# Kernel optimization log

Hardware: AMD Instinct MI355X
Metric: run time of the kernel (lower is better)

Reference implementation:

```python
import jax, jax.numpy as jnp
import numpy as np

K = 7          # involution kernel size
P = 3          # padding = (K-1)//2
GC = 16        # group_channels in involution
EPS = 1e-5


def bn(x, g, b):
    # training-mode BatchNorm2d forward: per-channel batch stats over (B,H,W)
    m = jnp.mean(x, axis=(0, 2, 3), keepdims=True)
    v = jnp.var(x, axis=(0, 2, 3), keepdims=True)
    return (x - m) * jax.lax.rsqrt(v + EPS) * g[None, :, None, None] + b[None, :, None, None]


def conv1x1(x, w):
    # x: [B,C,H,W], w: [O,C] -> [B,O,H,W]
    return jnp.einsum('bchw,oc->bohw', x, w)


def unfold7(x):
    # torch F.unfold(kernel=7, pad=3, stride=1) -> [B, C, K*K, H, W] (C slowest, matching torch layout)
    B, C, H, W = x.shape
    xp = jnp.pad(x, ((0, 0), (0, 0), (P, P), (P, P)))
    return jnp.stack([xp[:, :, i:i + H, j:j + W] for i in range(K) for j in range(K)], axis=2)


def involution(x, wr, gr, br, ws):
    # kernel generation: 1x1 reduce -> BN -> ReLU -> 1x1 span to G*K*K per-pixel kernels
    B, C, H, W = x.shape
    G = C // GC
    t = jax.nn.relu(bn(conv1x1(x, wr), gr, br))          # [B, C//4, H, W]
    w = conv1x1(t, ws).reshape(B, G, 1, K * K, H, W)     # per-pixel kernels
    p = unfold7(x).reshape(B, G, GC, K * K, H, W)        # unfolded patches
    return jnp.sum(w * p, axis=3).reshape(B, C, H, W)    # multiply-accumulate over K*K


def setup_inputs() -> dict:
    key = jax.random.key(0)
    ks = jax.random.split(key, 14)
    Cin, Cout, mid = 256, 256, 64
    red = mid // 4                 # reduction_ratio = 4
    G = mid // GC                  # groups = 4
    s = lambda *sh: 1.0 / np.sqrt(np.prod(sh[1:]) if len(sh) > 1 else sh[0])
    return {
        'x':  jax.random.normal(ks[0], (8, Cin, 56, 56), jnp.float32),
        'w1': jax.random.normal(ks[1], (mid, Cin), jnp.float32) * s(mid, Cin),
        'g1': jnp.ones((mid,), jnp.float32),
        'b1': jnp.zeros((mid,), jnp.float32),
        'wr': jax.random.normal(ks[2], (red, mid), jnp.float32) * s(red, mid),
        'gr': jnp.ones((red,), jnp.float32),
        'br': jnp.zeros((red,), jnp.float32),
        'ws': jax.random.normal(ks[3], (K * K * G, red), jnp.float32) * s(K * K * G, red),
        'g2': jnp.ones((mid,), jnp.float32),
        'b2': jnp.zeros((mid,), jnp.float32),
        'w3': jax.random.normal(ks[4], (Cout, mid), jnp.float32) * s(Cout, mid),
        'g3': jnp.ones((Cout,), jnp.float32),
        'b3': jnp.zeros((Cout,), jnp.float32),
    }


def reference(x, w1, g1, b1, wr, gr, br, ws, g2, b2, w3, g3, b3):
    out = jax.nn.relu(bn(conv1x1(x, w1), g1, b1))        # conv1 1x1 + BN + ReLU
    out = jax.nn.relu(bn(involution(out, wr, gr, br, ws), g2, b2))  # involution + BN + ReLU
    out = bn(conv1x1(out, w3), g3, b3)                   # conv3 1x1 + BN
    return jax.nn.relu(out + x)                          # residual add + ReLU
```

## Files before the change

### kernel.cpp

```cpp
#include <hip/hip_runtime.h>

#define HW 3136
#define NPIX 25088
#define NBLK 392

#define OFF_Y1   0u
#define OFF_TR   1605632u
#define OFF_WT   2007040u
#define OFF_OUT2 6924288u
#define OFF_Y3   8529920u
#define OFF_ST   14952448u
#define ACC1 0
#define ACCR 128
#define ACC2 160
#define ACC3 288
#define FIN1 800
#define FINR 928
#define FIN2 960
#define FIN3 1088

__device__ __forceinline__ float wave_sum(float v) {
    #pragma unroll
    for (int off = 32; off > 0; off >>= 1) v += __shfl_xor(v, off, 64);
    return v;
}

__global__ __launch_bounds__(256) void k_wt(const float* __restrict__ w1,
        const float* __restrict__ w3, float* __restrict__ w1t, float* __restrict__ w3t) {
    int i = blockIdx.x * 256 + threadIdx.x;
    if (i < 16384) {
        int oc = i >> 8, ic = i & 255;
        w1t[ic * 64 + oc] = w1[i];
    } else {
        int j = i - 16384;
        int oc = j >> 6, ic = j & 63;
        w3t[ic * 256 + oc] = w3[j];
    }
}

__global__ __launch_bounds__(256, 2) void k_conv1(const float* __restrict__ x,
        const float* __restrict__ w1t, float* __restrict__ y1, float* __restrict__ st) {
    __shared__ float ws[256][32];
    int t = threadIdx.x, blk = blockIdx.x;
    int oh = blk & 1, pb = blk >> 1;
    int b = pb / 49, hw0 = (pb % 49) * 64;
    int tx = t & 15, ty = t >> 4;
    #pragma unroll
    for (int i = 0; i < 8; i++) {
        int e = i * 256 + t;
        int ic = e >> 3, c4 = e & 7;
        *(float4*)&ws[ic][c4 * 4] = *(const float4*)&w1t[ic * 64 + oh * 32 + c4 * 4];
    }
    __syncthreads();
    float a00 = 0.f, a01 = 0.f, a02 = 0.f, a03 = 0.f;
    float a10 = 0.f, a11 = 0.f, a12 = 0.f, a13 = 0.f;
    const float* xp = x + (size_t)b * 256 * HW + hw0 + tx * 4;
    #pragma unroll 8
    for (int ic = 0; ic < 256; ic++) {
        float4 xv = *(const float4*)(xp + (size_t)ic * HW);
        float2 wv = *(const float2*)&ws[ic][ty * 2];
        a00 = fmaf(wv.x, xv.x, a00); a01 = fmaf(wv.x, xv.y, a01);
        a02 = fmaf(wv.x, xv.z, a02); a03 = fmaf(wv.x, xv.w, a03);
        a10 = fmaf(wv.y, xv.x, a10); a11 = fmaf(wv.y, xv.y, a11);
        a12 = fmaf(wv.y, xv.z, a12); a13 = fmaf(wv.y, xv.w, a13);
    }
    #pragma unroll
    for (int io = 0; io < 2; io++) {
        int oc = oh * 32 + ty * 2 + io;
        float4 o = io ? make_float4(a10, a11, a12, a13) : make_float4(a00, a01, a02, a03);
        *(float4*)&y1[((b * 64) + oc) * HW + hw0 + tx * 4] = o;
        float s = o.x + o.y + o.z + o.w;
        float q = o.x * o.x + o.y * o.y + o.z * o.z + o.w * o.w;
        #pragma unroll
        for (int off = 1; off <= 8; off <<= 1) {
            s += __shfl_xor(s, off, 64);
            q += __shfl_xor(q, off, 64);
        }
        if (tx == 0) {
            atomicAdd(&st[ACC1 + oc], s);
            atomicAdd(&st[ACC1 + 64 + oc], q);
        }
    }
}

__global__ void k_fin(const float* __restrict__ acc, float* __restrict__ fin,
                      const float* __restrict__ gamma, const float* __restrict__ beta, int C) {
    int c = threadIdx.x;
    if (c < C) {
        float mean = acc[c] * (1.0f / (float)NPIX);
        float var  = acc[C + c] * (1.0f / (float)NPIX) - mean * mean;
        float rstd = rsqrtf(var + 1e-5f);
        float a = gamma[c] * rstd;
        fin[c] = a;
        fin[C + c] = beta[c] - mean * a;
    }
}

__global__ __launch_bounds__(256, 4) void k_bn1_convr(float* __restrict__ y1,
        const float* __restrict__ wr, float* __restrict__ tr, float* __restrict__ st) {
    __shared__ float ys[64][64];
    __shared__ float wsh[16][64];
    int t = threadIdx.x, pb = blockIdx.x;
    int b = pb / 49, hw0 = (pb % 49) * 64;
    int tx = t & 15, ty = t >> 4;
    #pragma unroll
    for (int i = 0; i < 16; i++) {
        int e = i * 256 + t, c = e >> 6, p = e & 63;
        int gi = ((b * 64) + c) * HW + hw0 + p;
        float v = y1[gi];
        v = fmaxf(st[FIN1 + c] * v + st[FIN1 + 64 + c], 0.f);
        ys[c][p] = v;
        y1[gi] = v;
    }
    #pragma unroll
    for (int i = 0; i < 4; i++) {
        int e = i * 256 + t;
        wsh[e >> 6][e & 63] = wr[e];
    }
    __syncthreads();
    float a0 = 0.f, a1 = 0.f, a2 = 0.f, a3 = 0.f;
    #pragma unroll 8
    for (int c = 0; c < 64; c++) {
        float4 yv = *(const float4*)&ys[c][tx * 4];
        float wv = wsh[ty][c];
        a0 = fmaf(wv, yv.x, a0); a1 = fmaf(wv, yv.y, a1);
        a2 = fmaf(wv, yv.z, a2); a3 = fmaf(wv, yv.w, a3);
    }
    *(float4*)&tr[((b * 16) + ty) * HW + hw0 + tx * 4] = make_float4(a0, a1, a2, a3);
    float s = a0 + a1 + a2 + a3;
    float q = a0 * a0 + a1 * a1 + a2 * a2 + a3 * a3;
    #pragma unroll
    for (int off = 1; off <= 8; off <<= 1) {
        s += __shfl_xor(s, off, 64);
        q += __shfl_xor(q, off, 64);
    }
    if (tx == 0) {
        atomicAdd(&st[ACCR + ty], s);
        atomicAdd(&st[ACCR + 16 + ty], q);
    }
}

__global__ __launch_bounds__(256) void k_invol(const float* __restrict__ y1r,
        const float* __restrict__ tr, const float* __restrict__ wsp,
        float* __restrict__ out2, float* __restrict__ st) {
    __shared__ float ts[16][256];
    __shared__ float sw[49][16];
    __shared__ float ps[8][10][64];
    __shared__ float red[4][16];
    int t = threadIdx.x, bidx = blockIdx.x;
    int h = bidx & 1, r2 = bidx >> 1;
    int ht = r2 % 14;
    int bg = r2 / 14;
    int g = bg & 3, b = bg >> 2;
    int h0 = ht * 4;
    int c0 = h * 8;
    #pragma unroll
    for (int i = 0; i < 16; i++) {
        int e = i * 256 + t, c = e >> 8, p = e & 255;
        if (p < 224) {
            float v = tr[((b * 16) + c) * HW + h0 * 56 + p];
            ts[c][p] = fmaxf(st[FINR + c] * v + st[FINR + 16 + c], 0.f);
        }
    }
    for (int e = t; e < 784; e += 256) sw[e >> 4][e & 15] = wsp[g * 784 + e];
    for (int i = 0; i < 20; i++) {
        int e = i * 256 + t;
        int c = e / 640, rem = e - c * 640;
        int r = rem >> 6, wc = rem & 63;
        int gh = h0 + r - 3, gw = wc - 3;
        float v = 0.f;
        if (gh >= 0 && gh < 56 && gw >= 0 && gw < 56)
            v = y1r[((b * 64) + g * 16 + c0 + c) * HW + gh * 56 + gw];
        ps[c][r][wc] = v;
    }
    __syncthreads();
    float accv[8];
    #pragma unroll
    for (int c = 0; c < 8; c++) accv[c] = 0.f;
    bool active = t < 224;
    if (active) {
        int lh = t / 56, lw = t % 56;
        float tsr[16];
        #pragma unroll
        for (int c = 0; c < 16; c++) tsr[c] = ts[c][t];
        float kr[49];
        #pragma unroll
        for (int k = 0; k < 49; k++) {
            const float4* swr = (const float4*)&sw[k][0];
            float4 u0 = swr[0], u1 = swr[1], u2 = swr[2], u3 = swr[3];
            float v = u0.x * tsr[0];
            v = fmaf(u0.y, tsr[1], v);  v = fmaf(u0.z, tsr[2], v);  v = fmaf(u0.w, tsr[3], v);
            v = fmaf(u1.x, tsr[4], v);  v = fmaf(u1.y, tsr[5], v);  v = fmaf(u1.z, tsr[6], v);
            v = fmaf(u1.w, tsr[7], v);  v = fmaf(u2.x, tsr[8], v);  v = fmaf(u2.y, tsr[9], v);
            v = fmaf(u2.z, tsr[10], v); v = fmaf(u2.w, tsr[11], v); v = fmaf(u3.x, tsr[12], v);
            v = fmaf(u3.y, tsr[13], v); v = fmaf(u3.z, tsr[14], v); v = fmaf(u3.w, tsr[15], v);
            kr[k] = v;
        }
        #pragma unroll
        for (int k = 0; k < 49; k++) {
            int ki = k / 7, kj = k % 7;
            float kv = kr[k];
            #pragma unroll
            for (int c = 0; c < 8; c++)
                accv[c] = fmaf(kv, ps[c][lh + ki][lw + kj], accv[c]);
        }
        int hw = h0 * 56 + t;
        #pragma unroll
        for (int c = 0; c < 8; c++)
            out2[((b * 64) + g * 16 + c0 + c) * HW + hw] = accv[c];
    }
    int wave = t >> 6, lane = t & 63;
    #pragma unroll
    for (int c = 0; c < 8; c++) {
        float v = active ? accv[c] : 0.f;
        float s  = wave_sum(v);
        float s2 = wave_sum(v * v);
        if (lane == 0) { red[wave][c] = s; red[wave][8 + c] = s2; }
    }
    __syncthreads();
    if (t < 16) {
        float s = red[0][t] + red[1][t] + red[2][t] + red[3][t];
        int c = t & 7, isq = t >> 3;
        atomicAdd(&st[ACC2 + isq * 64 + g * 16 + c0 + c], s);
    }
}

__global__ __launch_bounds__(256, 4) void k_bn2_conv3(const float* __restrict__ out2,
        const float* __restrict__ w3t, float* __restrict__ y3, float* __restrict__ st) {
    __shared__ float os[64][64];
    __shared__ float wst[64][64];
    int t = threadIdx.x, blk = blockIdx.x;
    int occ = blk & 3, pb = blk >> 2;
    int b = pb / 49, hw0 = (pb % 49) * 64;
    int tx = t & 15, ty = t >> 4;
    #pragma unroll
    for (int i = 0; i < 16; i++) {
        int e = i * 256 + t, c = e >> 6, p = e & 63;
        float v = out2[((b * 64) + c) * HW + hw0 + p];
        os[c][p] = fmaxf(st[FIN2 + c] * v + st[FIN2 + 64 + c], 0.f);
        wst[c][p] = w3t[c * 256 + occ * 64 + p];
    }
    __syncthreads();
    float acc[4][4];
    #pragma unroll
    for (int i = 0; i < 4; i++)
        #pragma unroll
        for (int j = 0; j < 4; j++) acc[i][j] = 0.f;
    #pragma unroll 8
    for (int c = 0; c < 64; c++) {
        float4 xv = *(const float4*)&os[c][tx * 4];
        float4 wv = *(const float4*)&wst[c][ty * 4];
        float xa[4] = {xv.x, xv.y, xv.z, xv.w};
        float wa[4] = {wv.x, wv.y, wv.z, wv.w};
        #pragma unroll
        for (int i = 0; i < 4; i++)
            #pragma unroll
            for (int j = 0; j < 4; j++) acc[i][j] = fmaf(wa[i], xa[j], acc[i][j]);
    }
    #pragma unroll
    for (int i = 0; i < 4; i++) {
        int oc = occ * 64 + ty * 4 + i;
        float4 o = make_float4(acc[i][0], acc[i][1], acc[i][2], acc[i][3]);
        *(float4*)&y3[((b * 256) + oc) * HW + hw0 + tx * 4] = o;
        float s = o.x + o.y + o.z + o.w;
        float q = o.x * o.x + o.y * o.y + o.z * o.z + o.w * o.w;
        #pragma unroll
        for (int off = 1; off <= 8; off <<= 1) {
            s += __shfl_xor(s, off, 64);
            q += __shfl_xor(q, off, 64);
        }
        if (tx == 0) {
            atomicAdd(&st[ACC3 + oc], s);
            atomicAdd(&st[ACC3 + 256 + oc], q);
        }
    }
}

__global__ __launch_bounds__(256) void k_final(const float* __restrict__ y3,
        const float* __restrict__ x, float* __restrict__ out, const float* __restrict__ st) {
    int idx = blockIdx.x * 256 + threadIdx.x;
    if (idx < 1605632) {
        int c = (idx / 784) & 255;
        float a = st[FIN3 + c], bb = st[FIN3 + 256 + c];
        float4 v  = ((const float4*)y3)[idx];
        float4 xv = ((const float4*)x)[idx];
        float4 o;
        o.x = fmaxf(a * v.x + bb + xv.x, 0.f);
        o.y = fmaxf(a * v.y + bb + xv.y, 0.f);
        o.z = fmaxf(a * v.z + bb + xv.z, 0.f);
        o.w = fmaxf(a * v.w + bb + xv.w, 0.f);
        ((float4*)out)[idx] = o;
    }
}

extern "C" void kernel_launch(void* const* d_in, const int* in_sizes, int n_in,
                              void* d_out, int out_size, void* d_ws, size_t ws_size,
                              hipStream_t stream) {
    const float* x   = (const float*)d_in[0];
    const float* w1  = (const float*)d_in[1];
    const float* g1  = (const float*)d_in[2];
    const float* b1  = (const float*)d_in[3];
    const float* wr  = (const float*)d_in[4];
    const float* gr  = (const float*)d_in[5];
    const float* br  = (const float*)d_in[6];
    const float* wsp = (const float*)d_in[7];
    const float* g2  = (const float*)d_in[8];
    const float* b2  = (const float*)d_in[9];
    const float* w3  = (const float*)d_in[10];
    const float* g3  = (const float*)d_in[11];
    const float* b3  = (const float*)d_in[12];
    float* out = (float*)d_out;
    float* w   = (float*)d_ws;
    float* y1   = w + OFF_Y1;
    float* tr   = w + OFF_TR;
    float* w1t  = w + OFF_WT;
    float* w3t  = w + OFF_WT + 16384;
    float* out2 = w + OFF_OUT2;
    float* y3   = w + OFF_Y3;
    float* st   = w + OFF_ST;

    hipMemsetAsync(st, 0, 2048 * sizeof(float), stream);
    k_wt<<<128, 256, 0, stream>>>(w1, w3, w1t, w3t);
    k_conv1<<<NBLK * 2, 256, 0, stream>>>(x, w1t, y1, st);
    k_fin<<<1, 64, 0, stream>>>(st + ACC1, st + FIN1, g1, b1, 64);
    k_bn1_convr<<<NBLK, 256, 0, stream>>>(y1, wr, tr, st);
    k_fin<<<1, 64, 0, stream>>>(st + ACCR, st + FINR, gr, br, 16);
    k_invol<<<896, 256, 0, stream>>>(y1, tr, wsp, out2, st);
    k_fin<<<1, 64, 0, stream>>>(st + ACC2, st + FIN2, g2, b2, 64);
    k_bn2_conv3<<<NBLK * 4, 256, 0, stream>>>(out2, w3t, y3, st);
    k_fin<<<1, 256, 0, stream>>>(st + ACC3, st + FIN3, g3, b3, 256);
    k_final<<<6272, 256, 0, stream>>>(y3, x, out, st);
}
```

Before: 293.3 us.

## Retile conv1 with shared-memory x/w tiles, 4x4 register blocking and prefetch

Rewrites the first 1x1 convolution so each 128-thread block computes all 64 output channels for 32 pixels. Input channels are processed in chunks of 64, and both x and weights are staged through shared memory. Each thread now holds a 4x4 accumulator tile, and the next chunk is prefetched into registers while the current one is computed. Before, each block covered only half the output channels, so x was read from global memory twice; this change removes that duplicate read and raises arithmetic intensity. The cost is more registers and extra syncthreads per chunk.

New measurement: 332.0 us. 13.2% more time.

```diff
diff --git a/kernel.cpp b/kernel.cpp
--- a/kernel.cpp
+++ b/kernel.cpp
@@ -38,41 +38,80 @@
     }
 }
 
-__global__ __launch_bounds__(256, 2) void k_conv1(const float* __restrict__ x,
+__global__ __launch_bounds__(128, 4) void k_conv1(const float* __restrict__ x,
         const float* __restrict__ w1t, float* __restrict__ y1, float* __restrict__ st) {
-    __shared__ float ws[256][32];
-    int t = threadIdx.x, blk = blockIdx.x;
-    int oh = blk & 1, pb = blk >> 1;
-    int b = pb / 49, hw0 = (pb % 49) * 64;
-    int tx = t & 15, ty = t >> 4;
+    __shared__ float xs[64][32];
+    __shared__ float ws[64][64];
+    int t = threadIdx.x, pb = blockIdx.x;
+    int b = pb / 98, hw0 = (pb % 98) * 32;
+    int tx = t & 7, ty = t >> 3;
+    const size_t xbase = (size_t)(b * 256) * HW + hw0;
+
+    float4 px[4], pw[8];
+    #pragma unroll
+    for (int i = 0; i < 4; i++) {
+        int e = i * 128 + t, ic = e >> 3, p4 = e & 7;
+        px[i] = *(const float4*)&x[xbase + (size_t)ic * HW + p4 * 4];
+    }
     #pragma unroll
     for (int i = 0; i < 8; i++) {
-        int e = i * 256 + t;
-        int ic = e >> 3, c4 = e & 7;
-        *(float4*)&ws[ic][c4 * 4] = *(const float4*)&w1t[ic * 64 + oh * 32 + c4 * 4];
-    }
-    __syncthreads();
-    float a00 = 0.f, a01 = 0.f, a02 = 0.f, a03 = 0.f;
-    float a10 = 0.f, a11 = 0.f, a12 = 0.f, a13 = 0.f;
-    const float* xp = x + (size_t)b * 256 * HW + hw0 + tx * 4;
-    #pragma unroll 8
-    for (int ic = 0; ic < 256; ic++) {
-        float4 xv = *(const float4*)(xp + (size_t)ic * HW);
-        float2 wv = *(const float2*)&ws[ic][ty * 2];
-        a00 = fmaf(wv.x, xv.x, a00); a01 = fmaf(wv.x, xv.y, a01);
-        a02 = fmaf(wv.x, xv.z, a02); a03 = fmaf(wv.x, xv.w, a03);
-        a10 = fmaf(wv.y, xv.x, a10); a11 = fmaf(wv.y, xv.y, a11);
-        a12 = fmaf(wv.y, xv.z, a12); a13 = fmaf(wv.y, xv.w, a13);
-    }
-    #pragma unroll
-    for (int io = 0; io < 2; io++) {
-        int oc = oh * 32 + ty * 2 + io;
-        float4 o = io ? make_float4(a10, a11, a12, a13) : make_float4(a00, a01, a02, a03);
+        int e = i * 128 + t, ic = e >> 4, q = e & 15;
+        pw[i] = *(const float4*)&w1t[ic * 64 + q * 4];
+    }
+
+    float acc[4][4];
+    #pragma unroll
+    for (int i = 0; i < 4; i++)
+        #pragma unroll
+        for (int j = 0; j < 4; j++) acc[i][j] = 0.f;
+
+    #pragma unroll 1
+    for (int cc = 0; cc < 4; cc++) {
+        #pragma unroll
+        for (int i = 0; i < 4; i++) {
+            int e = i * 128 + t, ic = e >> 3, p4 = e & 7;
+            *(float4*)&xs[ic][p4 * 4] = px[i];
+        }
+        #pragma unroll
+        for (int i = 0; i < 8; i++) {
+            int e = i * 128 + t, ic = e >> 4, q = e & 15;
+            *(float4*)&ws[ic][q * 4] = pw[i];
+        }
+        __syncthreads();
+        if (cc < 3) {
+            #pragma unroll
+            for (int i = 0; i < 4; i++) {
+                int e = i * 128 + t, ic = e >> 3, p4 = e & 7;
+                px[i] = *(const float4*)&x[xbase + (size_t)((cc + 1) * 64 + ic) * HW + p4 * 4];
+            }
+            #pragma unroll
+            for (int i = 0; i < 8; i++) {
+                int e = i * 128 + t, ic = e >> 4, q = e & 15;
+                pw[i] = *(const float4*)&w1t[((cc + 1) * 64 + ic) * 64 + q * 4];
+            }
+        }
+        #pragma unroll 8
+        for (int c = 0; c < 64; c++) {
+            float4 xv = *(const float4*)&xs[c][tx * 4];
+            float4 wv = *(const float4*)&ws[c][ty * 4];
+            float xa[4] = {xv.x, xv.y, xv.z, xv.w};
+            float wa[4] = {wv.x, wv.y, wv.z, wv.w};
+            #pragma unroll
+            for (int i = 0; i < 4; i++)
+                #pragma unroll
+                for (int j = 0; j < 4; j++) acc[i][j] = fmaf(wa[i], xa[j], acc[i][j]);
+        }
+        __syncthreads();
+    }
+    #pragma unroll
+    for (int i = 0; i < 4; i++) {
+        int oc = ty * 4 + i;
+        float4 o = make_float4(acc[i][0], acc[i][1], acc[i][2], acc[i][3]);
         *(float4*)&y1[((b * 64) + oc) * HW + hw0 + tx * 4] = o;
         float s = o.x + o.y + o.z + o.w;
         float q = o.x * o.x + o.y * o.y + o.z * o.z + o.w * o.w;
         #pragma unroll
-        for (int off = 1; off <= 8; off <<= 1) {
+        for (int off = 1; off <= 4; off <<= 1) {
             s += __shfl_xor(s, off, 64);
             q += __shfl_xor(q, off, 64);
         }
@@ -321,7 +360,7 @@
 
     hipMemsetAsync(st, 0, 2048 * sizeof(float), stream);
     k_wt<<<128, 256, 0, stream>>>(w1, w3, w1t, w3t);
-    k_conv1<<<NBLK * 2, 256, 0, stream>>>(x, w1t, y1, st);
+    k_conv1<<<784, 128, 0, stream>>>(x, w1t, y1, st);
     k_fin<<<1, 64, 0, stream>>>(st + ACC1, st + FIN1, g1, b1, 64);
     k_bn1_convr<<<NBLK, 256, 0, stream>>>(y1, wr, tr, st);
     k_fin<<<1, 64, 0, stream>>>(st + ACCR, st + FINR, gr, br, 16);
```

## Enlarge per-thread register tiles in conv1 and conv3 to cut redundant input reads

Applied to the files above, without the earlier changes.

conv1 now has each block compute all 64 output channels, with a 4x4 register tile per thread, instead of splitting output channels across two blocks. As a result x is read from global memory once instead of twice. conv3 now covers 128 output channels per block with an 8x4 tile per thread, streaming out2 directly from global memory and applying BN2+ReLU in registers rather than staging it in shared memory, so out2 is read twice instead of four times. The trade-off is fewer blocks, higher register pressure and lower occupancy, plus the BN affine being recomputed per channel read.

Result: slower. 326.7 us (+11.4%).

```diff
diff --git a/kernel.cpp b/kernel.cpp
--- a/kernel.cpp
+++ b/kernel.cpp
@@ -38,36 +38,40 @@
     }
 }
 
-__global__ __launch_bounds__(256, 2) void k_conv1(const float* __restrict__ x,
+__global__ __launch_bounds__(256) void k_conv1(const float* __restrict__ x,
         const float* __restrict__ w1t, float* __restrict__ y1, float* __restrict__ st) {
-    __shared__ float ws[256][32];
-    int t = threadIdx.x, blk = blockIdx.x;
-    int oh = blk & 1, pb = blk >> 1;
+    __shared__ float ws[256][64];
+    int t = threadIdx.x, pb = blockIdx.x;
     int b = pb / 49, hw0 = (pb % 49) * 64;
     int tx = t & 15, ty = t >> 4;
     #pragma unroll
-    for (int i = 0; i < 8; i++) {
+    for (int i = 0; i < 16; i++) {
         int e = i * 256 + t;
-        int ic = e >> 3, c4 = e & 7;
-        *(float4*)&ws[ic][c4 * 4] = *(const float4*)&w1t[ic * 64 + oh * 32 + c4 * 4];
-    }
-    __syncthreads();
-    float a00 = 0.f, a01 = 0.f, a02 = 0.f, a03 = 0.f;
-    float a10 = 0.f, a11 = 0.f, a12 = 0.f, a13 = 0.f;
-    const float* xp = x + (size_t)b * 256 * HW + hw0 + tx * 4;
+        int ic = e >> 4, q = e & 15;
+        *(float4*)&ws[ic][q * 4] = *(const float4*)&w1t[ic * 64 + q * 4];
+    }
+    __syncthreads();
+    float acc[4][4];
+    #pragma unroll
+    for (int i = 0; i < 4; i++)
+        #pragma unroll
+        for (int j = 0; j < 4; j++) acc[i][j] = 0.f;
+    const float* xp = x + (size_t)(b * 256) * HW + hw0 + tx * 4;
     #pragma unroll 8
     for (int ic = 0; ic < 256; ic++) {
         float4 xv = *(const float4*)(xp + (size_t)ic * HW);
-        float2 wv = *(const float2*)&ws[ic][ty * 2];
-        a00 = fmaf(wv.x, xv.x, a00); a01 = fmaf(wv.x, xv.y, a01);
-        a02 = fmaf(wv.x, xv.z, a02); a03 = fmaf(wv.x, xv.w, a03);
-        a10 = fmaf(wv.y, xv.x, a10); a11 = fmaf(wv.y, xv.y, a11);
-        a12 = fmaf(wv.y, xv.z, a12); a13 = fmaf(wv.y, xv.w, a13);
-    }
-    #pragma unroll
-    for (int io = 0; io < 2; io++) {
-        int oc = oh * 32 + ty * 2 + io;
-        float4 o = io ? make_float4(a10, a11, a12, a13) : make_float4(a00, a01, a02, a03);
+        float4 wv = *(const float4*)&ws[ic][ty * 4];
+        float xa[4] = {xv.x, xv.y, xv.z, xv.w};
+        float wa[4] = {wv.x, wv.y, wv.z, wv.w};
+        #pragma unroll
+        for (int i = 0; i < 4; i++)
+            #pragma unroll
+            for (int j = 0; j < 4; j++) acc[i][j] = fmaf(wa[i], xa[j], acc[i][j]);
+    }
+    #pragma unroll
+    for (int i = 0; i < 4; i++) {
+        int oc = ty * 4 + i;
+        float4 o = make_float4(acc[i][0], acc[i][1], acc[i][2], acc[i][3]);
         *(float4*)&y1[((b * 64) + oc) * HW + hw0 + tx * 4] = o;
         float s = o.x + o.y + o.z + o.w;
         float q = o.x * o.x + o.y * o.y + o.z * o.z + o.w * o.w;
@@ -225,41 +229,46 @@
     }
 }
 
-__global__ __launch_bounds__(256, 4) void k_bn2_conv3(const float* __restrict__ out2,
+__global__ __launch_bounds__(256) void k_bn2_conv3(const float* __restrict__ out2,
         const float* __restrict__ w3t, float* __restrict__ y3, float* __restrict__ st) {
-    __shared__ float os[64][64];
-    __shared__ float wst[64][64];
+    __shared__ float ws[64][128];
     int t = threadIdx.x, blk = blockIdx.x;
-    int occ = blk & 3, pb = blk >> 2;
+    int oh = blk & 1, pb = blk >> 1;
     int b = pb / 49, hw0 = (pb % 49) * 64;
     int tx = t & 15, ty = t >> 4;
     #pragma unroll
-    for (int i = 0; i < 16; i++) {
-        int e = i * 256 + t, c = e >> 6, p = e & 63;
-        float v = out2[((b * 64) + c) * HW + hw0 + p];
-        os[c][p] = fmaxf(st[FIN2 + c] * v + st[FIN2 + 64 + c], 0.f);
-        wst[c][p] = w3t[c * 256 + occ * 64 + p];
-    }
-    __syncthreads();
-    float acc[4][4];
-    #pragma unroll
-    for (int i = 0; i < 4; i++)
+    for (int i = 0; i < 8; i++) {
+        int e = i * 256 + t;
+        int ic = e >> 5, q = e & 31;
+        *(float4*)&ws[ic][q * 4] = *(const float4*)&w3t[ic * 256 + oh * 128 + q * 4];
+    }
+    __syncthreads();
+    float acc[8][4];
+    #pragma unroll
+    for (int i = 0; i < 8; i++)
         #pragma unroll
         for (int j = 0; j < 4; j++) acc[i][j] = 0.f;
+    const float* xp = out2 + (size_t)(b * 64) * HW + hw0 + tx * 4;
     #pragma unroll 8
-    for (int c = 0; c < 64; c++) {
-        float4 xv = *(const float4*)&os[c][tx * 4];
-        float4 wv = *(const float4*)&wst[c][ty * 4];
-        float xa[4] = {xv.x, xv.y, xv.z, xv.w};
-        float wa[4] = {wv.x, wv.y, wv.z, wv.w};
-        #pragma unroll
-        for (int i = 0; i < 4; i++)
+    for (int ic = 0; ic < 64; ic++) {
+        float4 xv = *(const float4*)(xp + (size_t)ic * HW);
+        float fa = st[FIN2 + ic], fb = st[FIN2 + 64 + ic];
+        float xa[4];
+        xa[0] = fmaxf(fmaf(fa, xv.x, fb), 0.f);
+        xa[1] = fmaxf(fmaf(fa, xv.y, fb), 0.f);
+        xa[2] = fmaxf(fmaf(fa, xv.z, fb), 0.f);
+        xa[3] = fmaxf(fmaf(fa, xv.w, fb), 0.f);
+        float4 wv0 = *(const float4*)&ws[ic][ty * 8];
+        float4 wv1 = *(const float4*)&ws[ic][ty * 8 + 4];
+        float wa[8] = {wv0.x, wv0.y, wv0.z, wv0.w, wv1.x, wv1.y, wv1.z, wv1.w};
+        #pragma unroll
+        for (int i = 0; i < 8; i++)
             #pragma unroll
             for (int j = 0; j < 4; j++) acc[i][j] = fmaf(wa[i], xa[j], acc[i][j]);
     }
     #pragma unroll
-    for (int i = 0; i < 4; i++) {
-        int oc = occ * 64 + ty * 4 + i;
+    for (int i = 0; i < 8; i++) {
+        int oc = oh * 128 + ty * 8 + i;
         float4 o = make_float4(acc[i][0], acc[i][1], acc[i][2], acc[i][3]);
         *(float4*)&y3[((b * 256) + oc) * HW + hw0 + tx * 4] = o;
         float s = o.x + o.y + o.z + o.w;
@@ -321,13 +330,13 @@
 
     hipMemsetAsync(st, 0, 2048 * sizeof(float), stream);
     k_wt<<<128, 256, 0, stream>>>(w1, w3, w1t, w3t);
-    k_conv1<<<NBLK * 2, 256, 0, stream>>>(x, w1t, y1, st);
+    k_conv1<<<NBLK, 256, 0, stream>>>(x, w1t, y1, st);
     k_fin<<<1, 64, 0, stream>>>(st + ACC1, st + FIN1, g1, b1, 64);
     k_bn1_convr<<<NBLK, 256, 0, stream>>>(y1, wr, tr, st);
     k_fin<<<1, 64, 0, stream>>>(st + ACCR, st + FINR, gr, br, 16);
     k_invol<<<896, 256, 0, stream>>>(y1, tr, wsp, out2, st);
     k_fin<<<1, 64, 0, stream>>>(st + ACC2, st + FIN2, g2, b2, 64);
-    k_bn2_conv3<<<NBLK * 4, 256, 0, stream>>>(out2, w3t, y3, st);
+    k_bn2_conv3<<<NBLK * 2, 256, 0, stream>>>(out2, w3t, y3, st);
     k_fin<<<1, 256, 0, stream>>>(st + ACC3, st + FIN3, g3, b3, 256);
     k_final<<<6272, 256, 0, stream>>>(y3, x, out, st);
 }
```

## Tile conv1 with double-buffered LDS via global_load_lds and recompute BN1 in involution

Applied to the files above, without the earlier changes.

Conv1 now stages 64-channel chunks of x and the transposed weights into double-buffered LDS with direct global-to-LDS loads. Each thread computes a 4x4 register tile covering all 64 output channels, so x is read once per pixel block instead of twice. Separately, the BN1+ReLU result is no longer written back to y1; the involution kernel applies BN1+ReLU on the fly while loading patches. This removes one full read-modify-write of y1 but adds per-element BN math on the overlapping halo loads.

Measured after the change: 275.1 us. 1.07x faster.

```diff
diff --git a/kernel.cpp b/kernel.cpp
--- a/kernel.cpp
+++ b/kernel.cpp
@@ -25,6 +25,12 @@
     return v;
 }
 
+__device__ __forceinline__ void gl_lds16(const float* g, float* l) {
+    __builtin_amdgcn_global_load_lds(
+        (const __attribute__((address_space(1))) unsigned int*)g,
+        (__attribute__((address_space(3))) unsigned int*)l, 16, 0, 0);
+}
+
 __global__ __launch_bounds__(256) void k_wt(const float* __restrict__ w1,
         const float* __restrict__ w3, float* __restrict__ w1t, float* __restrict__ w3t) {
     int i = blockIdx.x * 256 + threadIdx.x;
@@ -38,36 +44,55 @@
     }
 }
 
-__global__ __launch_bounds__(256, 2) void k_conv1(const float* __restrict__ x,
+__global__ __launch_bounds__(256) void k_conv1(const float* __restrict__ x,
         const float* __restrict__ w1t, float* __restrict__ y1, float* __restrict__ st) {
-    __shared__ float ws[256][32];
-    int t = threadIdx.x, blk = blockIdx.x;
-    int oh = blk & 1, pb = blk >> 1;
+    __shared__ float xs[2][64][64];
+    __shared__ float ws[2][64][64];
+    int t = threadIdx.x, pb = blockIdx.x;
     int b = pb / 49, hw0 = (pb % 49) * 64;
     int tx = t & 15, ty = t >> 4;
-    #pragma unroll
-    for (int i = 0; i < 8; i++) {
-        int e = i * 256 + t;
-        int ic = e >> 3, c4 = e & 7;
-        *(float4*)&ws[ic][c4 * 4] = *(const float4*)&w1t[ic * 64 + oh * 32 + c4 * 4];
-    }
-    __syncthreads();
-    float a00 = 0.f, a01 = 0.f, a02 = 0.f, a03 = 0.f;
-    float a10 = 0.f, a11 = 0.f, a12 = 0.f, a13 = 0.f;
-    const float* xp = x + (size_t)b * 256 * HW + hw0 + tx * 4;
-    #pragma unroll 8
-    for (int ic = 0; ic < 256; ic++) {
-        float4 xv = *(const float4*)(xp + (size_t)ic * HW);
-        float2 wv = *(const float2*)&ws[ic][ty * 2];
-        a00 = fmaf(wv.x, xv.x, a00); a01 = fmaf(wv.x, xv.y, a01);
-        a02 = fmaf(wv.x, xv.z, a02); a03 = fmaf(wv.x, xv.w, a03);
-        a10 = fmaf(wv.y, xv.x, a10); a11 = fmaf(wv.y, xv.y, a11);
-        a12 = fmaf(wv.y, xv.z, a12); a13 = fmaf(wv.y, xv.w, a13);
-    }
-    #pragma unroll
-    for (int io = 0; io < 2; io++) {
-        int oc = oh * 32 + ty * 2 + io;
-        float4 o = io ? make_float4(a10, a11, a12, a13) : make_float4(a00, a01, a02, a03);
+    int wv = t >> 6, ln = t & 63;
+
+    #define STAGE(cc, buf)                                                        \
+        _Pragma("unroll")                                                         \
+        for (int i = 0; i < 4; i++) {                                             \
+            int s = i * 4 + wv;                                                   \
+            const float* gx = x + (size_t)((b * 256) + (cc) * 64 + s * 4 + (ln >> 4)) * HW \
+                              + hw0 + (ln & 15) * 4;                              \
+            gl_lds16(gx, &xs[buf][s * 4][0]);                                     \
+            const float* gw = w1t + ((cc) * 64 + s * 4) * 64 + ln * 4;            \
+            gl_lds16(gw, &ws[buf][s * 4][0]);                                     \
+        }
+
+    STAGE(0, 0);
+    __syncthreads();
+    float acc[4][4];
+    #pragma unroll
+    for (int i = 0; i < 4; i++)
+        #pragma unroll
+        for (int j = 0; j < 4; j++) acc[i][j] = 0.f;
+    #pragma unroll 1
+    for (int cc = 0; cc < 4; cc++) {
+        int cur = cc & 1;
+        if (cc < 3) STAGE(cc + 1, cur ^ 1);
+        #pragma unroll 8
+        for (int c = 0; c < 64; c++) {
+            float4 xv = *(const float4*)&xs[cur][c][tx * 4];
+            float4 wv4 = *(const float4*)&ws[cur][c][ty * 4];
+            float xa[4] = {xv.x, xv.y, xv.z, xv.w};
+            float wa[4] = {wv4.x, wv4.y, wv4.z, wv4.w};
+            #pragma unroll
+            for (int i = 0; i < 4; i++)
+                #pragma unroll
+                for (int j = 0; j < 4; j++) acc[i][j] = fmaf(wa[i], xa[j], acc[i][j]);
+        }
+        __syncthreads();
+    }
+    #undef STAGE
+    #pragma unroll
+    for (int i = 0; i < 4; i++) {
+        int oc = ty * 4 + i;
+        float4 o = make_float4(acc[i][0], acc[i][1], acc[i][2], acc[i][3]);
         *(float4*)&y1[((b * 64) + oc) * HW + hw0 + tx * 4] = o;
         float s = o.x + o.y + o.z + o.w;
         float q = o.x * o.x + o.y * o.y + o.z * o.z + o.w * o.w;
@@ -96,7 +121,7 @@
     }
 }
 
-__global__ __launch_bounds__(256, 4) void k_bn1_convr(float* __restrict__ y1,
+__global__ __launch_bounds__(256, 4) void k_bn1_convr(const float* __restrict__ y1,
         const float* __restrict__ wr, float* __restrict__ tr, float* __restrict__ st) {
     __shared__ float ys[64][64];
     __shared__ float wsh[16][64];
@@ -106,11 +131,8 @@
     #pragma unroll
     for (int i = 0; i < 16; i++) {
         int e = i * 256 + t, c = e >> 6, p = e & 63;
-        int gi = ((b * 64) + c) * HW + hw0 + p;
-        float v = y1[gi];
-        v = fmaxf(st[FIN1 + c] * v + st[FIN1 + 64 + c], 0.f);
-        ys[c][p] = v;
-        y1[gi] = v;
+        float v = y1[((b * 64) + c) * HW + hw0 + p];
+        ys[c][p] = fmaxf(st[FIN1 + c] * v + st[FIN1 + 64 + c], 0.f);
     }
     #pragma unroll
     for (int i = 0; i < 4; i++) {
@@ -140,7 +162,7 @@
     }
 }
 
-__global__ __launch_bounds__(256) void k_invol(const float* __restrict__ y1r,
+__global__ __launch_bounds__(256) void k_invol(const float* __restrict__ y1,
         const float* __restrict__ tr, const float* __restrict__ wsp,
         float* __restrict__ out2, float* __restrict__ st) {
     __shared__ float ts[16][256];
@@ -169,8 +191,11 @@
         int r = rem >> 6, wc = rem & 63;
         int gh = h0 + r - 3, gw = wc - 3;
         float v = 0.f;
-        if (gh >= 0 && gh < 56 && gw >= 0 && gw < 56)
-            v = y1r[((b * 64) + g * 16 + c0 + c) * HW + gh * 56 + gw];
+        if (gh >= 0 && gh < 56 && gw >= 0 && gw < 56) {
+            int ch = g * 16 + c0 + c;
+            float raw = y1[((b * 64) + ch) * HW + gh * 56 + gw];
+            v = fmaxf(st[FIN1 + ch] * raw + st[FIN1 + 64 + ch], 0.f);
+        }
         ps[c][r][wc] = v;
     }
     __syncthreads();
@@ -321,7 +346,7 @@
 
     hipMemsetAsync(st, 0, 2048 * sizeof(float), stream);
     k_wt<<<128, 256, 0, stream>>>(w1, w3, w1t, w3t);
-    k_conv1<<<NBLK * 2, 256, 0, stream>>>(x, w1t, y1, st);
+    k_conv1<<<NBLK, 256, 0, stream>>>(x, w1t, y1, st);
     k_fin<<<1, 64, 0, stream>>>(st + ACC1, st + FIN1, g1, b1, 64);
     k_bn1_convr<<<NBLK, 256, 0, stream>>>(y1, wr, tr, st);
     k_fin<<<1, 64, 0, stream>>>(st + ACCR, st + FINR, gr, br, 16);
```
